# Optimization experiments

Hardware: AMD Instinct MI355X
Metric: run time of the kernel (lower is better)

The kernel has to match this reference:

```python
import jax, jax.numpy as jnp
import numpy as np

# db4 decomposition low-pass filter (pywt convention, 8 taps)
DEC_LO = np.array([-0.010597401784997278, 0.032883011666982945, 0.030841381835986965,
                   -0.18703481171888114, -0.02798376941698385, 0.6308807679295904,
                   0.7148465705525415, 0.23037781330885523], dtype=np.float32)
L = DEC_LO.shape[0]  # 8
REC_LO = DEC_LO[::-1].copy()
DEC_HI = (REC_LO * ((-1.0) ** (np.arange(L) + 1))).astype(np.float32)
REC_HI = DEC_HI[::-1].copy()
LEVEL = 7

# lax.conv does correlation; flip filters to get true convolution (pywt semantics)
K_DEC = jnp.asarray(np.stack([DEC_LO[::-1], DEC_HI[::-1]])[:, None, :])  # [2,1,L] out-ch: (lo, hi)
K_REC = jnp.asarray(np.stack([REC_LO[::-1], REC_HI[::-1]])[None, :, :])  # [1,2,L] in-ch: (ca, cd)


def dwt(x):
    # x: [B, N]. pywt zero-mode dwt == full conv then take odd indices;
    # fused here as stride-2 conv with asymmetric padding (L-2, L-1).
    y = jax.lax.conv_general_dilated(x[:, None, :], K_DEC, (2,), [(L - 2, L - 1)])
    return y[:, 0], y[:, 1]  # each [B, floor((N+L-1)/2)]


def idwt(ca, cd):
    # upsample-by-2 (lhs_dilation, length 2n-1), full conv, trim L-2 each side -> pad (1,1)
    y = jax.lax.conv_general_dilated(jnp.stack([ca, cd], axis=1), K_REC, (1,),
                                     [(1, 1)], lhs_dilation=(2,))
    return y[:, 0]  # [B, 2n - L + 2]


def soft(c, t):
    # pywt.threshold(mode='soft')
    return jnp.sign(c) * jnp.maximum(jnp.abs(c) - t, 0.0)


def setup_inputs() -> dict:
    key = jax.random.key(0)
    k1, k2 = jax.random.split(key)
    x = jax.random.normal(k1, (32768, 1116), dtype=jnp.float32)
    # learned scalar parameter, initialized like nn.Parameter(torch.tensor(0.02))
    raw_threshold = jnp.asarray(0.02, dtype=jnp.float32)
    return {"x": x, "raw_threshold": raw_threshold}


def reference(x, raw_threshold):
    thr = jnp.maximum(raw_threshold, 0.01)  # torch.clamp(min=0.01)
    # wavedec: 7-level analysis
    a = x
    details = []
    for _ in range(LEVEL):
        a, d = dwt(a)
        details.append(d)
    # soft-threshold every coefficient band (including approximation)
    a = soft(a, thr)
    details = [soft(d, thr) for d in details]
    # waverec: synthesis, truncating cA when one sample longer than cD (pywt rule)
    for d in reversed(details):
        if a.shape[-1] > d.shape[-1]:
            a = a[:, : d.shape[-1]]
        a = idwt(a, d)
    return a  # [B, 1116]
```

## Files before the change

### kernel.cpp

```cpp
#include <hip/hip_runtime.h>

#define NCOL 1116
#define NLEV 7
#define NT 64
#define ARENA 2048
#define NRPW 2

namespace {
constexpr float DEC_LO[8] = {-0.010597401784997278f,  0.032883011666982945f,
                              0.030841381835986965f, -0.18703481171888114f,
                             -0.02798376941698385f,   0.6308807679295904f,
                              0.7148465705525415f,    0.23037781330885523f};
constexpr float DEC_HI[8] = {-0.23037781330885523f,   0.7148465705525415f,
                             -0.6308807679295904f,   -0.02798376941698385f,
                              0.18703481171888114f,   0.030841381835986965f,
                             -0.032883011666982945f, -0.010597401784997278f};
constexpr float REC_LO[8] = { 0.23037781330885523f,   0.7148465705525415f,
                              0.6308807679295904f,   -0.02798376941698385f,
                             -0.18703481171888114f,   0.030841381835986965f,
                              0.032883011666982945f, -0.010597401784997278f};
constexpr float REC_HI[8] = {-0.010597401784997278f, -0.032883011666982945f,
                              0.030841381835986965f,  0.18703481171888114f,
                             -0.02798376941698385f,  -0.6308807679295904f,
                              0.7148465705525415f,   -0.23037781330885523f};
constexpr int alen[8] = {1116, 561, 284, 145, 76, 41, 24, 15};
constexpr int doff[7] = {0, 562, 846, 992, 1068, 1110, 1134};
}

static __device__ __forceinline__ float softf(float c, float t) {
    return copysignf(fmaxf(fabsf(c) - t, 0.0f), c);
}

static __device__ __forceinline__ void dec8(const float* v, float& lo, float& hi) {
    float l = DEC_LO[7] * v[0];
    float h = DEC_HI[7] * v[0];
    #pragma unroll
    for (int s = 6; s >= 0; --s) {
        l = fmaf(DEC_LO[s], v[7 - s], l);
        h = fmaf(DEC_HI[s], v[7 - s], h);
    }
    lo = l; hi = h;
}

static __device__ __forceinline__ float2 rec_pair(float ca0, float ca1, float ca2, float ca3,
                                                  float cd0, float cd1, float cd2, float cd3) {
    float y0 = fmaf(REC_LO[0], ca3, fmaf(REC_LO[2], ca2, fmaf(REC_LO[4], ca1, REC_LO[6] * ca0)));
    y0 = fmaf(REC_HI[0], cd3, fmaf(REC_HI[2], cd2, fmaf(REC_HI[4], cd1, fmaf(REC_HI[6], cd0, y0))));
    float y1 = fmaf(REC_LO[1], ca3, fmaf(REC_LO[3], ca2, fmaf(REC_LO[5], ca1, REC_LO[7] * ca0)));
    y1 = fmaf(REC_HI[1], cd3, fmaf(REC_HI[3], cd2, fmaf(REC_HI[5], cd1, fmaf(REC_HI[7], cd0, y1))));
    return make_float2(y0, y1);
}

__global__ __launch_bounds__(NT)
void wavelet_kernel(const float* __restrict__ x,
                    const float* __restrict__ thr_ptr,
                    float* __restrict__ out, int nrow) {
    __shared__ __align__(16) float SH[NRPW * ARENA];

    const int lane = threadIdx.x;
    const int row0 = blockIdx.x * NRPW;
    if (row0 >= nrow) return;
    const int rows[2] = {row0, min(row0 + 1, nrow - 1)};

    const float thr = fmaxf(thr_ptr[0], 0.01f);

    float* dpool[NRPW]; float* b8[NRPW]; float* c8[NRPW];
    #pragma unroll
    for (int r = 0; r < NRPW; ++r) {
        float* a = SH + r * ARENA;
        dpool[r] = a;
        b8[r]    = a + 1156;
        c8[r]    = a + 1732;
    }

    {
        const float* xr[NRPW] = {x + (size_t)rows[0] * NCOL, x + (size_t)rows[1] * NCOL};
        #pragma unroll
        for (int k = 0; k < 9; ++k) {
            const int o = lane + (k << 6);
            if (k < 8 || lane < 49) {
                #pragma unroll
                for (int r = 0; r < NRPW; ++r) {
                    float v[8];
                    bool fast = (k >= 1 && k <= 7);
                    if (!fast) fast = (o >= 3 && o <= 557);
                    if (fast) {
                        const float2* p = (const float2*)(xr[r] + 2 * o - 6);
                        float2 q0 = p[0], q1 = p[1], q2 = p[2], q3 = p[3];
                        v[0] = q0.x; v[1] = q0.y; v[2] = q1.x; v[3] = q1.y;
                        v[4] = q2.x; v[5] = q2.y; v[6] = q3.x; v[7] = q3.y;
                    } else {
                        #pragma unroll
                        for (int j = 0; j < 8; ++j) {
                            const int idx = 2 * o - 6 + j;
                            v[j] = (idx >= 0 && idx < NCOL) ? xr[r][idx] : 0.0f;
                        }
                    }
                    float lo, hi;
                    dec8(v, lo, hi);
                    b8[r][o]    = lo;
                    dpool[r][o] = softf(hi, thr);
                }
            }
        }
        #pragma unroll
        for (int r = 0; r < NRPW; ++r)
            if (lane < 14) { const int j = lane < 6 ? lane - 6 : 555 + lane; b8[r][j] = 0.0f; }
        __builtin_amdgcn_wave_barrier();
    }

    #pragma unroll
    for (int l = 1; l < NLEV; ++l) {
        const int nout = alen[l + 1];
        const int K = (nout + 63) >> 6;
        const int tailn = nout - ((K - 1) << 6);
        #pragma unroll
        for (int k = 0; k < K; ++k) {
            const int o = lane + (k << 6);
            if (k < K - 1 || lane < tailn) {
                #pragma unroll
                for (int r = 0; r < NRPW; ++r) {
                    float* const cur = (l & 1) ? b8[r] : c8[r];
                    float* const nxt = (l & 1) ? c8[r] : b8[r];
                    const float2* p = (const float2*)(cur + 2 * o - 6);
                    float2 q0 = p[0], q1 = p[1], q2 = p[2], q3 = p[3];
                    float v[8] = {q0.x, q0.y, q1.x, q1.y, q2.x, q2.y, q3.x, q3.y};
                    float lo, hi;
                    dec8(v, lo, hi);
                    nxt[o] = (l == NLEV - 1) ? softf(lo, thr) : lo;
                    (dpool[r] + doff[l])[o] = softf(hi, thr);
                }
            }
        }
        if (l < NLEV - 1) {
            #pragma unroll
            for (int r = 0; r < NRPW; ++r)
                if (lane < 14) {
                    const int j = lane < 6 ? lane - 6 : nout + lane - 6;
                    ((l & 1) ? c8[r] : b8[r])[j] = 0.0f;
                }
        }
        __builtin_amdgcn_wave_barrier();
    }

    #pragma unroll
    for (int l = NLEV - 1; l >= 1; --l) {
        const int M = alen[l + 1];
        const int npair = M - 3;
        const int Qf = npair >> 1;
        const int KI = (Qf + 63) >> 6;
        const int tailq = Qf - ((KI - 1) << 6);
        #pragma unroll
        for (int k = 0; k < KI; ++k) {
            const int q = lane + (k << 6);
            if (k < KI - 1 || lane < tailq) {
                const int m = q << 1;
                #pragma unroll
                for (int r = 0; r < NRPW; ++r) {
                    const float* const cur = (l & 1) ? c8[r] : b8[r];
                    float* const nxt       = (l & 1) ? b8[r] : c8[r];
                    const float* const dp  = dpool[r] + doff[l];
                    const float2* pa = (const float2*)(cur + m);
                    const float2* pd = (const float2*)(dp + m);
                    float2 a01 = pa[0], a23 = pa[1];
                    float2 d01 = pd[0], d23 = pd[1];
                    float ca4 = cur[m + 4], cd4 = dp[m + 4];
                    float2 y01 = rec_pair(a01.x, a01.y, a23.x, a23.y, d01.x, d01.y, d23.x, d23.y);
                    float2 y23 = rec_pair(a01.y, a23.x, a23.y, ca4, d01.y, d23.x, d23.y, cd4);
                    *(float4*)(nxt + 2 * m) = make_float4(y01.x, y01.y, y23.x, y23.y);
                }
            }
        }
        if ((npair & 1) && lane == 0) {
            const int m = npair - 1;
            #pragma unroll
            for (int r = 0; r < NRPW; ++r) {
                const float* const cur = (l & 1) ? c8[r] : b8[r];
                float* const nxt       = (l & 1) ? b8[r] : c8[r];
                const float* const dp  = dpool[r] + doff[l];
                float2 y01 = rec_pair(cur[m], cur[m + 1], cur[m + 2], cur[m + 3],
                                      dp[m],  dp[m + 1],  dp[m + 2],  dp[m + 3]);
                *(float2*)(nxt + 2 * m) = y01;
            }
        }
        __builtin_amdgcn_wave_barrier();
    }

    {
        float4* orow[NRPW] = {(float4*)(out + (size_t)rows[0] * NCOL),
                              (float4*)(out + (size_t)rows[1] * NCOL)};
        #pragma unroll
        for (int k = 0; k < 5; ++k) {
            const int q = lane + (k << 6);
            if (k < 4 || lane < 23) {
                const int m = q << 1;
                #pragma unroll
                for (int r = 0; r < NRPW; ++r) {
                    const float* const cur = b8[r];
                    const float* const dp  = dpool[r];
                    const float2* pa = (const float2*)(cur + m);
                    const float2* pd = (const float2*)(dp + m);
                    float2 a01 = pa[0], a23 = pa[1];
                    float2 d01 = pd[0], d23 = pd[1];
                    float ca4 = cur[m + 4], cd4 = dp[m + 4];
                    float2 y01 = rec_pair(a01.x, a01.y, a23.x, a23.y, d01.x, d01.y, d23.x, d23.y);
                    float2 y23 = rec_pair(a01.y, a23.x, a23.y, ca4, d01.y, d23.x, d23.y, cd4);
                    orow[r][q] = make_float4(y01.x, y01.y, y23.x, y23.y);
                }
            }
        }
    }
}

extern "C" void kernel_launch(void* const* d_in, const int* in_sizes, int n_in,
                              void* d_out, int out_size, void* d_ws, size_t ws_size,
                              hipStream_t stream) {
    const float* x = (const float*)d_in[0];
    const float* thr = (const float*)d_in[1];
    float* out = (float*)d_out;
    const int nrow = in_sizes[0] / NCOL;
    const int nblk = (nrow + NRPW - 1) / NRPW;
    hipLaunchKernelGGL(wavelet_kernel, dim3(nblk), dim3(NT), 0, stream, x, thr, out, nrow);
}
```

Measured before the change: 283.8 us.

## Spill intermediate wavelet bands to output row to shrink LDS per row

Reduces shared memory per row from a 2048-float arena to 1184 by storing detail bands of levels 1-4 and one ping-pong approximation buffer in the row's own output slice in global memory. The output row is overwritten at the end, so it serves as scratch. Each block now runs four waves, one row per wave, instead of one wave handling two rows. The aim is higher occupancy from the smaller LDS footprint, at the cost of extra global/L2 traffic and vmcnt drains between levels.

```diff
diff --git a/kernel.cpp b/kernel.cpp
--- a/kernel.cpp
+++ b/kernel.cpp
@@ -2,9 +2,12 @@
 
 #define NCOL 1116
 #define NLEV 7
-#define NT 64
-#define ARENA 2048
-#define NRPW 2
+#define NT 256
+#define RPB 4
+#define ARENA 1184
+
+#define WB() __builtin_amdgcn_wave_barrier()
+#define VDRAIN() asm volatile("s_waitcnt vmcnt(0)" ::: "memory")
 
 namespace {
 constexpr float DEC_LO[8] = {-0.010597401784997278f,  0.032883011666982945f,
@@ -23,8 +26,6 @@
                               0.030841381835986965f,  0.18703481171888114f,
                              -0.02798376941698385f,  -0.6308807679295904f,
                               0.7148465705525415f,   -0.23037781330885523f};
-constexpr int alen[8] = {1116, 561, 284, 145, 76, 41, 24, 15};
-constexpr int doff[7] = {0, 562, 846, 992, 1068, 1110, 1134};
 }
 
 static __device__ __forceinline__ float softf(float c, float t) {
@@ -51,162 +52,149 @@
     return make_float2(y0, y1);
 }
 
+template<int NOUT, bool SOFT_A>
+static __device__ __forceinline__ void fwd_level(const float* __restrict__ cur,
+                                                 float* __restrict__ nxt,
+                                                 float* __restrict__ dW,
+                                                 int lane, float thr) {
+    constexpr int K = (NOUT + 63) >> 6;
+    constexpr int TAIL = NOUT - ((K - 1) << 6);
+    #pragma unroll
+    for (int k = 0; k < K; ++k) {
+        const int o = lane + (k << 6);
+        if (k < K - 1 || lane < TAIL) {
+            const float2* p = (const float2*)(cur + 2 * o - 6);
+            float2 q0 = p[0], q1 = p[1], q2 = p[2], q3 = p[3];
+            float v[8] = {q0.x, q0.y, q1.x, q1.y, q2.x, q2.y, q3.x, q3.y};
+            float lo, hi;
+            dec8(v, lo, hi);
+            nxt[o] = SOFT_A ? softf(lo, thr) : lo;
+            dW[o]  = softf(hi, thr);
+        }
+    }
+}
+
+template<int M>
+static __device__ __forceinline__ void inv_level(const float* __restrict__ cur,
+                                                 const float* __restrict__ dp,
+                                                 float* __restrict__ nxt, int lane) {
+    constexpr int npair = M - 3;
+    constexpr int Qf = npair >> 1;
+    constexpr int KI = (Qf + 63) >> 6;
+    constexpr int TAILQ = Qf - ((KI - 1) << 6);
+    #pragma unroll
+    for (int k = 0; k < KI; ++k) {
+        const int q = lane + (k << 6);
+        if (k < KI - 1 || lane < TAILQ) {
+            const int m = q << 1;
+            const float2* pa = (const float2*)(cur + m);
+            const float2* pd = (const float2*)(dp + m);
+            float2 a01 = pa[0], a23 = pa[1];
+            float2 d01 = pd[0], d23 = pd[1];
+            float ca4 = cur[m + 4], cd4 = dp[m + 4];
+            float2 y01 = rec_pair(a01.x, a01.y, a23.x, a23.y, d01.x, d01.y, d23.x, d23.y);
+            float2 y23 = rec_pair(a01.y, a23.x, a23.y, ca4, d01.y, d23.x, d23.y, cd4);
+            *(float4*)(nxt + 2 * m) = make_float4(y01.x, y01.y, y23.x, y23.y);
+        }
+    }
+    if constexpr (npair & 1) {
+        if (lane == 0) {
+            const int m = npair - 1;
+            float2 y01 = rec_pair(cur[m], cur[m + 1], cur[m + 2], cur[m + 3],
+                                  dp[m],  dp[m + 1],  dp[m + 2],  dp[m + 3]);
+            *(float2*)(nxt + 2 * m) = y01;
+        }
+    }
+}
+
+static __device__ __forceinline__ void pads(float* base, int nout, int lane) {
+    if (lane < 14) { const int j = lane < 6 ? lane - 6 : nout + lane - 6; base[j] = 0.0f; }
+}
+
 __global__ __launch_bounds__(NT)
 void wavelet_kernel(const float* __restrict__ x,
                     const float* __restrict__ thr_ptr,
                     float* __restrict__ out, int nrow) {
-    __shared__ __align__(16) float SH[NRPW * ARENA];
-
-    const int lane = threadIdx.x;
-    const int row0 = blockIdx.x * NRPW;
-    if (row0 >= nrow) return;
-    const int rows[2] = {row0, min(row0 + 1, nrow - 1)};
+    __shared__ __align__(16) float SH[RPB * ARENA];
+
+    const int lane = threadIdx.x & 63;
+    const int wv   = threadIdx.x >> 6;
+    const int row  = blockIdx.x * RPB + wv;
+    if (row >= nrow) return;
 
     const float thr = fmaxf(thr_ptr[0], 0.01f);
 
-    float* dpool[NRPW]; float* b8[NRPW]; float* c8[NRPW];
-    #pragma unroll
-    for (int r = 0; r < NRPW; ++r) {
-        float* a = SH + r * ARENA;
-        dpool[r] = a;
-        b8[r]    = a + 1156;
-        c8[r]    = a + 1732;
-    }
+    float* const arena = SH + wv * ARENA;
+    float* const lD0 = arena;
+    float* const lD5 = arena + 562;
+    float* const lD6 = arena + 586;
+    float* const lB  = arena + 608;
+
+    float* const orow = out + (size_t)row * NCOL;
+    float* const gC   = orow + 556;
+    const float* const xrow = x + (size_t)row * NCOL;
 
     {
-        const float* xr[NRPW] = {x + (size_t)rows[0] * NCOL, x + (size_t)rows[1] * NCOL};
         #pragma unroll
         for (int k = 0; k < 9; ++k) {
             const int o = lane + (k << 6);
             if (k < 8 || lane < 49) {
-                #pragma unroll
-                for (int r = 0; r < NRPW; ++r) {
-                    float v[8];
-                    bool fast = (k >= 1 && k <= 7);
-                    if (!fast) fast = (o >= 3 && o <= 557);
-                    if (fast) {
-                        const float2* p = (const float2*)(xr[r] + 2 * o - 6);
-                        float2 q0 = p[0], q1 = p[1], q2 = p[2], q3 = p[3];
-                        v[0] = q0.x; v[1] = q0.y; v[2] = q1.x; v[3] = q1.y;
-                        v[4] = q2.x; v[5] = q2.y; v[6] = q3.x; v[7] = q3.y;
-                    } else {
-                        #pragma unroll
-                        for (int j = 0; j < 8; ++j) {
-                            const int idx = 2 * o - 6 + j;
-                            v[j] = (idx >= 0 && idx < NCOL) ? xr[r][idx] : 0.0f;
-                        }
+                float v[8];
+                bool fast = (k >= 1 && k <= 7);
+                if (!fast) fast = (o >= 3 && o <= 557);
+                if (fast) {
+                    const float2* p = (const float2*)(xrow + 2 * o - 6);
+                    float2 q0 = p[0], q1 = p[1], q2 = p[2], q3 = p[3];
+                    v[0] = q0.x; v[1] = q0.y; v[2] = q1.x; v[3] = q1.y;
+                    v[4] = q2.x; v[5] = q2.y; v[6] = q3.x; v[7] = q3.y;
+                } else {
+                    #pragma unroll
+                    for (int j = 0; j < 8; ++j) {
+                        const int idx = 2 * o - 6 + j;
+                        v[j] = (idx >= 0 && idx < NCOL) ? xrow[idx] : 0.0f;
                     }
-                    float lo, hi;
-                    dec8(v, lo, hi);
-                    b8[r][o]    = lo;
-                    dpool[r][o] = softf(hi, thr);
                 }
+                float lo, hi;
+                dec8(v, lo, hi);
+                lB[o]  = lo;
+                lD0[o] = softf(hi, thr);
             }
         }
-        #pragma unroll
-        for (int r = 0; r < NRPW; ++r)
-            if (lane < 14) { const int j = lane < 6 ? lane - 6 : 555 + lane; b8[r][j] = 0.0f; }
-        __builtin_amdgcn_wave_barrier();
-    }
-
-    #pragma unroll
-    for (int l = 1; l < NLEV; ++l) {
-        const int nout = alen[l + 1];
-        const int K = (nout + 63) >> 6;
-        const int tailn = nout - ((K - 1) << 6);
-        #pragma unroll
-        for (int k = 0; k < K; ++k) {
-            const int o = lane + (k << 6);
-            if (k < K - 1 || lane < tailn) {
-                #pragma unroll
-                for (int r = 0; r < NRPW; ++r) {
-                    float* const cur = (l & 1) ? b8[r] : c8[r];
-                    float* const nxt = (l & 1) ? c8[r] : b8[r];
-                    const float2* p = (const float2*)(cur + 2 * o - 6);
-                    float2 q0 = p[0], q1 = p[1], q2 = p[2], q3 = p[3];
-                    float v[8] = {q0.x, q0.y, q1.x, q1.y, q2.x, q2.y, q3.x, q3.y};
-                    float lo, hi;
-                    dec8(v, lo, hi);
-                    nxt[o] = (l == NLEV - 1) ? softf(lo, thr) : lo;
-                    (dpool[r] + doff[l])[o] = softf(hi, thr);
-                }
-            }
-        }
-        if (l < NLEV - 1) {
-            #pragma unroll
-            for (int r = 0; r < NRPW; ++r)
-                if (lane < 14) {
-                    const int j = lane < 6 ? lane - 6 : nout + lane - 6;
-                    ((l & 1) ? c8[r] : b8[r])[j] = 0.0f;
-                }
-        }
-        __builtin_amdgcn_wave_barrier();
-    }
-
-    #pragma unroll
-    for (int l = NLEV - 1; l >= 1; --l) {
-        const int M = alen[l + 1];
-        const int npair = M - 3;
-        const int Qf = npair >> 1;
-        const int KI = (Qf + 63) >> 6;
-        const int tailq = Qf - ((KI - 1) << 6);
-        #pragma unroll
-        for (int k = 0; k < KI; ++k) {
-            const int q = lane + (k << 6);
-            if (k < KI - 1 || lane < tailq) {
-                const int m = q << 1;
-                #pragma unroll
-                for (int r = 0; r < NRPW; ++r) {
-                    const float* const cur = (l & 1) ? c8[r] : b8[r];
-                    float* const nxt       = (l & 1) ? b8[r] : c8[r];
-                    const float* const dp  = dpool[r] + doff[l];
-                    const float2* pa = (const float2*)(cur + m);
-                    const float2* pd = (const float2*)(dp + m);
-                    float2 a01 = pa[0], a23 = pa[1];
-                    float2 d01 = pd[0], d23 = pd[1];
-                    float ca4 = cur[m + 4], cd4 = dp[m + 4];
-                    float2 y01 = rec_pair(a01.x, a01.y, a23.x, a23.y, d01.x, d01.y, d23.x, d23.y);
-                    float2 y23 = rec_pair(a01.y, a23.x, a23.y, ca4, d01.y, d23.x, d23.y, cd4);
-                    *(float4*)(nxt + 2 * m) = make_float4(y01.x, y01.y, y23.x, y23.y);
-                }
-            }
-        }
-        if ((npair & 1) && lane == 0) {
-            const int m = npair - 1;
-            #pragma unroll
-            for (int r = 0; r < NRPW; ++r) {
-                const float* const cur = (l & 1) ? c8[r] : b8[r];
-                float* const nxt       = (l & 1) ? b8[r] : c8[r];
-                const float* const dp  = dpool[r] + doff[l];
-                float2 y01 = rec_pair(cur[m], cur[m + 1], cur[m + 2], cur[m + 3],
-                                      dp[m],  dp[m + 1],  dp[m + 2],  dp[m + 3]);
-                *(float2*)(nxt + 2 * m) = y01;
-            }
-        }
-        __builtin_amdgcn_wave_barrier();
-    }
+        pads(lB, 561, lane);
+        WB();
+    }
+
+    fwd_level<284, false>(lB, gC, orow + 0,   lane, thr);  pads(gC, 284, lane); VDRAIN(); WB();
+    fwd_level<145, false>(gC, lB, orow + 284, lane, thr);  pads(lB, 145, lane);           WB();
+    fwd_level< 76, false>(lB, gC, orow + 430, lane, thr);  pads(gC,  76, lane); VDRAIN(); WB();
+    fwd_level< 41, false>(gC, lB, orow + 506, lane, thr);  pads(lB,  41, lane);           WB();
+    fwd_level< 24, false>(lB, gC, lD5,        lane, thr);  pads(gC,  24, lane); VDRAIN(); WB();
+    fwd_level< 15, true >(gC, lB, lD6,        lane, thr);                                 WB();
+
+    inv_level< 15>(lB, lD6,        gC, lane);  VDRAIN(); WB();
+    inv_level< 24>(gC, lD5,        lB, lane);            WB();
+    inv_level< 41>(lB, orow + 506, gC, lane);  VDRAIN(); WB();
+    inv_level< 76>(gC, orow + 430, lB, lane);            WB();
+    inv_level<145>(lB, orow + 284, gC, lane);  VDRAIN(); WB();
+    inv_level<284>(gC, orow + 0,   lB, lane);            WB();
 
     {
-        float4* orow[NRPW] = {(float4*)(out + (size_t)rows[0] * NCOL),
-                              (float4*)(out + (size_t)rows[1] * NCOL)};
+        const float* const cur = lB;
+        const float* const dp  = lD0;
+        float4* oq = (float4*)orow;
         #pragma unroll
         for (int k = 0; k < 5; ++k) {
             const int q = lane + (k << 6);
             if (k < 4 || lane < 23) {
                 const int m = q << 1;
-                #pragma unroll
-                for (int r = 0; r < NRPW; ++r) {
-                    const float* const cur = b8[r];
-                    const float* const dp  = dpool[r];
-                    const float2* pa = (const float2*)(cur + m);
-                    const float2* pd = (const float2*)(dp + m);
-                    float2 a01 = pa[0], a23 = pa[1];
-                    float2 d01 = pd[0], d23 = pd[1];
-                    float ca4 = cur[m + 4], cd4 = dp[m + 4];
-                    float2 y01 = rec_pair(a01.x, a01.y, a23.x, a23.y, d01.x, d01.y, d23.x, d23.y);
-                    float2 y23 = rec_pair(a01.y, a23.x, a23.y, ca4, d01.y, d23.x, d23.y, cd4);
-                    orow[r][q] = make_float4(y01.x, y01.y, y23.x, y23.y);
-                }
+                const float2* pa = (const float2*)(cur + m);
+                const float2* pd = (const float2*)(dp + m);
+                float2 a01 = pa[0], a23 = pa[1];
+                float2 d01 = pd[0], d23 = pd[1];
+                float ca4 = cur[m + 4], cd4 = dp[m + 4];
+                float2 y01 = rec_pair(a01.x, a01.y, a23.x, a23.y, d01.x, d01.y, d23.x, d23.y);
+                float2 y23 = rec_pair(a01.y, a23.x, a23.y, ca4, d01.y, d23.x, d23.y, cd4);
+                oq[q] = make_float4(y01.x, y01.y, y23.x, y23.y);
             }
         }
     }
@@ -219,6 +207,6 @@
     const float* thr = (const float*)d_in[1];
     float* out = (float*)d_out;
     const int nrow = in_sizes[0] / NCOL;
-    const int nblk = (nrow + NRPW - 1) / NRPW;
+    const int nblk = (nrow + RPB - 1) / RPB;
     hipLaunchKernelGGL(wavelet_kernel, dim3(nblk), dim3(NT), 0, stream, x, thr, out, nrow);
 }
```

After: 323.8 us. 14.1% more time.
